# Kernel optimization log

Measured on AMD Instinct MI355X. Metric: run time of the kernel, lower is better.

Reference implementation:

```python
import jax, jax.numpy as jnp
import numpy as np

N_ATOMS = 8192
MAX_NEIGHBORS = 12
MAX_RADIUS = 8.0
NUM_BINS = 50
WIDTH = 0.2


def setup_inputs() -> dict:
    key = jax.random.key(0)
    # uniform distances in [0,1): all within max_radius, so every node has
    # >= MAX_NEIGHBORS valid neighbors -> fixed output shape N*MAX_NEIGHBORS
    dm = jax.random.uniform(key, (N_ATOMS, N_ATOMS), dtype=jnp.float32)
    return {"distance_matrix": dm}


def reference(distance_matrix):
    n = distance_matrix.shape[0]
    # radius threshold: entries beyond max_radius are excluded from selection
    masked = jnp.where(distance_matrix <= MAX_RADius_const(), distance_matrix, jnp.inf) if False else jnp.where(distance_matrix <= MAX_RADIUS, distance_matrix, jnp.inf)
    # per-node smallest-k neighbors == original global-sort + per-node first-k
    _, nbr_idx = jax.lax.top_k(-masked, MAX_NEIGHBORS)  # [n, k]
    dists = jnp.take_along_axis(distance_matrix, nbr_idx, axis=1)  # [n, k]
    src = jnp.broadcast_to(jnp.arange(n, dtype=nbr_idx.dtype)[:, None], (n, MAX_NEIGHBORS))
    edge_index = jnp.stack([src, nbr_idx], axis=-1).reshape(-1, 2)  # [n*k, 2]
    # Gaussian RBF expansion
    centers = jnp.linspace(0.0, 1.0, NUM_BINS)  # [NUM_BINS]
    z = (dists[..., None] - centers) / WIDTH  # [n, k, NUM_BINS]
    edge_features = jnp.exp(-0.5 * z * z).reshape(-1, NUM_BINS)  # [n*k, NUM_BINS]
    return edge_index, edge_features
```

## Files before the change

### kernel.cpp

```cpp
#include <hip/hip_runtime.h>
#include <math.h>


#define N_ATOMS 8192
#define K 12
#define NBINS 50
#define CAP 256
#define WAVES 4
#define BLOCK (WAVES * 64)
#define MAX_RADIUS 8.0f
#define CAND_T 0.01f

__global__ __launch_bounds__(BLOCK) void edge_kernel(const float* __restrict__ dm,
                                                     float* __restrict__ out) {
    const int wave = threadIdx.x >> 6;
    const int lane = threadIdx.x & 63;
    const int row = blockIdx.x * WAVES + wave;
    const float* rowp = dm + (size_t)row * N_ATOMS;
    const float4* row4 = (const float4*)rowp;

    __shared__ unsigned long long s_keys[WAVES][CAP];
    __shared__ int s_selidx[WAVES][K];
    __shared__ float s_seldist[WAVES][K];

    const unsigned long long lane_below = (1ull << lane) - 1ull;

    int count = 0;
    #pragma unroll 4
    for (int i = 0; i < N_ATOMS / (64 * 4); ++i) {
        int v4 = lane + i * 64;
        float4 v = row4[v4];
        int bidx = v4 * 4;
        float vals[4] = {v.x, v.y, v.z, v.w};
        #pragma unroll
        for (int c = 0; c < 4; ++c) {
            float d = vals[c];
            bool pred = d < CAND_T;
            unsigned long long m = __ballot(pred);
            if (pred) {
                int pos = count + __popcll(m & lane_below);
                if (pos < CAP)
                    s_keys[wave][pos] =
                        ((unsigned long long)__float_as_uint(d) << 32) |
                        (unsigned int)(bidx + c);
            }
            count += __popcll(m);
        }
    }
    __syncthreads();

    if (count >= K && count <= CAP) {
        for (int j = lane; j < count; j += 64) {
            unsigned long long kj = s_keys[wave][j];
            int rank = 0;
            for (int m2 = 0; m2 < count; ++m2)
                rank += (s_keys[wave][m2] < kj) ? 1 : 0;
            if (rank < K) {
                s_selidx[wave][rank] = (int)(kj & 0xFFFFFFFFull);
                s_seldist[wave][rank] =
                    __uint_as_float((unsigned int)(kj >> 32));
            }
        }
    } else {
        unsigned long long last = 0ull;
        for (int r = 0; r < K; ++r) {
            unsigned long long best = ~0ull;
            for (int i = 0; i < N_ATOMS / (64 * 4); ++i) {
                int v4 = lane + i * 64;
                float4 v = row4[v4];
                int bidx = v4 * 4;
                float vals[4] = {v.x, v.y, v.z, v.w};
                #pragma unroll
                for (int c = 0; c < 4; ++c) {
                    float d = vals[c];
                    float md = (d <= MAX_RADIUS) ? d
                                                 : __uint_as_float(0x7F800000u);
                    unsigned long long key =
                        ((unsigned long long)__float_as_uint(md) << 32) |
                        (unsigned int)(bidx + c);
                    if (((r == 0) || (key > last)) && key < best) best = key;
                }
            }
            #pragma unroll
            for (int off = 32; off > 0; off >>= 1) {
                unsigned long long other = __shfl_xor(best, off, 64);
                if (other < best) best = other;
            }
            if (lane == 0) {
                int idx = (int)(best & 0xFFFFFFFFull);
                s_selidx[wave][r] = idx;
                s_seldist[wave][r] = rowp[idx];
            }
            last = best;
        }
    }

    float* out_ei = out;
    float* out_ef = out + (size_t)N_ATOMS * K * 2;
    if (lane < 2 * K) {
        int r = lane >> 1, comp = lane & 1;
        out_ei[((size_t)row * K + r) * 2 + comp] =
            comp ? (float)s_selidx[wave][r] : (float)row;
    }
    for (int t = lane; t < K * NBINS; t += 64) {
        int r = t / NBINS, b = t - r * NBINS;
        float d = s_seldist[wave][r];
        float z = (d - (float)b * (1.0f / 49.0f)) * 5.0f;
        out_ef[(size_t)row * K * NBINS + t] = __expf(-0.5f * z * z);
    }
}

extern "C" void kernel_launch(void* const* d_in, const int* in_sizes, int n_in,
                              void* d_out, int out_size, void* d_ws, size_t ws_size,
                              hipStream_t stream) {
    const float* dm = (const float*)d_in[0];
    float* out = (float*)d_out;
    edge_kernel<<<N_ATOMS / WAVES, BLOCK, 0, stream>>>(dm, out);
}
```

Before: 366.1 us.

## Replace per-element ballot compaction with per-lane candidate buffers and prefix-sum merge

The candidate filter no longer does a wave ballot and popcount for every element. Each lane now writes its own candidates into a private shared-memory slot of up to 12 entries. A wave-wide prefix scan then packs those slots into the shared key array. All 32 float4 loads per lane are issued in batches of 8 so more memory requests are in flight. The cost is a larger shared-memory footprint, which may reduce occupancy, and a fallback to the slow full-scan path whenever any lane overflows its slot.

Result: no change. 362.3 us (-1.0%).

```diff
diff --git a/kernel.cpp b/kernel.cpp
--- a/kernel.cpp
+++ b/kernel.cpp
@@ -5,7 +5,8 @@
 #define N_ATOMS 8192
 #define K 12
 #define NBINS 50
-#define CAP 256
+#define CAP 192
+#define CAP_LANE 12
 #define WAVES 4
 #define BLOCK (WAVES * 64)
 #define MAX_RADIUS 8.0f
@@ -19,41 +20,59 @@
     const float* rowp = dm + (size_t)row * N_ATOMS;
     const float4* row4 = (const float4*)rowp;
 
+    __shared__ unsigned long long s_lane[WAVES][64][CAP_LANE];
     __shared__ unsigned long long s_keys[WAVES][CAP];
     __shared__ int s_selidx[WAVES][K];
     __shared__ float s_seldist[WAVES][K];
 
-    const unsigned long long lane_below = (1ull << lane) - 1ull;
+    int cnt = 0;
+    #pragma unroll
+    for (int i = 0; i < 4; ++i) {
+        float4 v[8];
+        #pragma unroll
+        for (int j = 0; j < 8; ++j)
+            v[j] = row4[lane + (i * 8 + j) * 64];
+        #pragma unroll
+        for (int j = 0; j < 8; ++j) {
+            int bidx = (lane + (i * 8 + j) * 64) * 4;
+            float vals[4] = {v[j].x, v[j].y, v[j].z, v[j].w};
+            #pragma unroll
+            for (int c = 0; c < 4; ++c) {
+                float d = vals[c];
+                if (d < CAND_T) {
+                    if (cnt < CAP_LANE)
+                        s_lane[wave][lane][cnt] =
+                            ((unsigned long long)__float_as_uint(d) << 32) |
+                            (unsigned int)(bidx + c);
+                    cnt++;
+                }
+            }
+        }
+    }
 
-    int count = 0;
-    #pragma unroll 4
-    for (int i = 0; i < N_ATOMS / (64 * 4); ++i) {
-        int v4 = lane + i * 64;
-        float4 v = row4[v4];
-        int bidx = v4 * 4;
-        float vals[4] = {v.x, v.y, v.z, v.w};
-        #pragma unroll
-        for (int c = 0; c < 4; ++c) {
-            float d = vals[c];
-            bool pred = d < CAND_T;
-            unsigned long long m = __ballot(pred);
-            if (pred) {
-                int pos = count + __popcll(m & lane_below);
-                if (pos < CAP)
-                    s_keys[wave][pos] =
-                        ((unsigned long long)__float_as_uint(d) << 32) |
-                        (unsigned int)(bidx + c);
-            }
-            count += __popcll(m);
-        }
+    bool lane_ovf = cnt > CAP_LANE;
+    int stored = lane_ovf ? CAP_LANE : cnt;
+    int incl = stored;
+    #pragma unroll
+    for (int off = 1; off < 64; off <<= 1) {
+        int o = __shfl_up(incl, off, 64);
+        if (lane >= off) incl += o;
+    }
+    int excl = incl - stored;
+    int total = __shfl(incl, 63, 64);
+    bool ovf = __ballot(lane_ovf) != 0ull;
+
+    if (!ovf && total <= CAP) {
+        for (int t = 0; t < stored; ++t)
+            s_keys[wave][excl + t] = s_lane[wave][lane][t];
     }
     __syncthreads();
 
-    if (count >= K && count <= CAP) {
-        for (int j = lane; j < count; j += 64) {
+    if (!ovf && total >= K && total <= CAP) {
+        for (int j = lane; j < total; j += 64) {
             unsigned long long kj = s_keys[wave][j];
             int rank = 0;
-            for (int m2 = 0; m2 < count; ++m2)
+            for (int m2 = 0; m2 < total; ++m2)
                 rank += (s_keys[wave][m2] < kj) ? 1 : 0;
             if (rank < K) {
                 s_selidx[wave][rank] = (int)(kj & 0xFFFFFFFFull);
@@ -65,7 +84,7 @@
         unsigned long long last = 0ull;
         for (int r = 0; r < K; ++r) {
             unsigned long long best = ~0ull;
-            for (int i = 0; i < N_ATOMS / (64 * 4); ++i) {
+            for (int i = 0; i < 32; ++i) {
                 int v4 = lane + i * 64;
                 float4 v = row4[v4];
                 int bidx = v4 * 4;
```
